# Performance work log

Hardware: AMD Instinct MI355X
Metric: run time of the kernel (lower is better)

Reference implementation:

```python
import jax, jax.numpy as jnp
import numpy as np

N = 10000        # nodes
E = 320000       # edges (avg degree 32)
IN = 739         # in_channels
C = 64           # hid_channels
H = 1            # heads
D = C // H       # per-head dim
L = 10           # layer_num
G = 64           # num graphs in batch
LAMBD = 1.0


def setup_inputs() -> dict:
    key = jax.random.key(0)
    ks = jax.random.split(key, 14)
    s = 0.05
    return {
        "x": jax.random.normal(ks[0], (N, IN), jnp.float32),
        "edge_index": jax.random.randint(ks[1], (2, E), 0, N, dtype=jnp.int32),
        "batch": jnp.sort(jax.random.randint(ks[2], (N,), 0, G, dtype=jnp.int32)),
        # InitFeat: Linear(739->64), ELU, Linear(64->64) (dropout = identity at eval)
        "w0": jax.random.normal(ks[3], (IN, C), jnp.float32) * s,
        "b0": jax.random.normal(ks[4], (C,), jnp.float32) * s,
        "w1": jax.random.normal(ks[5], (C, C), jnp.float32) * s,
        "b1": jax.random.normal(ks[6], (C,), jnp.float32) * s,
        # AeroConv attention vectors for k = 1..L-1
        "conv_att": jax.random.normal(ks[7], (L - 1, H, D), jnp.float32) * s,
        # UpdateZ k=0 (g = h, width D) and k=1..L-1 (g = [h, z_scale], width 2D)
        "hop_att0": jax.random.normal(ks[8], (H, D), jnp.float32) * s,
        "hop_bias0": jax.random.normal(ks[9], (H,), jnp.float32) * s,
        "hop_att": jax.random.normal(ks[10], (L - 1, H, 2 * D), jnp.float32) * s,
        "hop_bias": jax.random.normal(ks[11], (L - 1, H), jnp.float32) * s,
        # readout head Linear(64->1)
        "w_head": jax.random.normal(ks[12], (C, 1), jnp.float32) * s,
        "b_head": jax.random.normal(ks[13], (1,), jnp.float32) * s,
    }


def reference(x, edge_index, batch, w0, b0, w1, b1, conv_att,
              hop_att0, hop_bias0, hop_att, hop_bias, w_head, b_head):
    src, dst = edge_index[0], edge_index[1]

    # ---- InitFeat (dropout is identity at inference) ----
    h = x @ w0 + b0
    h = jax.nn.elu(h) @ w1 + b1              # [N, C]
    x = h

    # ---- UpdateZ, k = 0: z = h * hop_attention ----
    hh = x.reshape(N, H, D)
    attn = jnp.sum(hop_att0 * jax.nn.elu(hh), axis=-1) + hop_bias0   # [N, H]
    z = hh * attn[..., None]                 # [N, H, D]

    for i in range(L - 1):
        k = i + 1
        scale = jnp.float32(np.log(LAMBD / k + 1.0 + 1e-6))
        z_scale = z * scale                  # [N, H, D]

        # per-edge attention: elu(z_i + z_j), dot with att, softplus
        a = jax.nn.elu(z_scale[src] + z_scale[dst])                   # [E, H, D]
        a = jax.nn.softplus(jnp.sum(conv_att[i] * a, axis=-1)) + 1e-6  # [E, H]

        # symmetric normalization by scatter-summed degree
        adj_sum = jax.ops.segment_sum(a, dst, num_segments=N)         # [N, H]
        inv = jnp.maximum(adj_sum, 1e-32) ** -0.5
        na = (inv[src] * a * inv[dst])[..., None]                     # [E, H, 1]

        # weighted scatter-sum of source features
        msgs = x[src].reshape(E, H, D) * na                           # [E, H, D]
        x = jax.ops.segment_sum(msgs, dst, num_segments=N).reshape(N, C)

        # UpdateZ (k >= 1): g = [h, z_scale]
        hh = x.reshape(N, H, D)
        g = jnp.concatenate([hh, z_scale], axis=-1)                   # [N, H, 2D]
        attn = jnp.sum(hop_att[i] * jax.nn.elu(g), axis=-1) + hop_bias[i]
        z = z + hh * attn[..., None]

    # ---- readout: elu, global mean pool over batch, linear head ----
    zf = jax.nn.elu(z.reshape(N, C))
    seg_sum = jax.ops.segment_sum(zf, batch, num_segments=G)          # [G, C]
    cnt = jax.ops.segment_sum(jnp.ones((N,), zf.dtype), batch, num_segments=G)
    pooled = seg_sum / jnp.maximum(cnt, 1.0)[:, None]
    return pooled @ w_head + b_head                                   # [G, 1]
```

## Files before the change

### kernel.cpp

```cpp
#include <hip/hip_runtime.h>
#include <hip/hip_bf16.h>
#include <math.h>

#define NN     10000
#define EE     320000
#define IN_CH  739
#define CC     64
#define GG     64
#define NLAYER 9
#define NBUCK  157
#define CHUNK  2048

__device__ __forceinline__ float eluf(float x) {
    return x > 0.f ? x : __expf(x) - 1.f;
}
__device__ __forceinline__ float softplusf(float x) {
    return fmaxf(x, 0.f) + __logf(1.f + __expf(-fabsf(x)));
}
__device__ __forceinline__ float wave_sum(float v) {
#pragma unroll
    for (int off = 32; off > 0; off >>= 1) v += __shfl_xor(v, off, 64);
    return v;
}

__device__ __forceinline__ int swizzle2500(int b) {
    const int r = b & 7;
    const int q = b >> 3;
    return r * 312 + (r < 4 ? r : 4) + q;
}

__global__ __launch_bounds__(256) void k_gemm1_part(
    const float* __restrict__ x, const float* __restrict__ w0,
    float* __restrict__ hpart)
{
    __shared__ float xs[64 * 68];
    __shared__ float ws[64 * 64];
    const int tid = threadIdx.x;
    const int cg_ = tid & 15;
    const int rg = tid >> 4;
    const int split = blockIdx.x & 3;
    const int R0 = (blockIdx.x >> 2) * 64;
    const int K0 = split * 192;

    const int sk = tid & 63;
    const int sr = tid >> 6;

    float xr[16], wr[16];
    float acc[4][4] = {};

#pragma unroll
    for (int i = 0; i < 16; ++i) {
        const int r = sr + 4 * i;
        const int gr = R0 + r;
        const int gk = K0 + sk;
        xr[i] = (gr < NN && gk < IN_CH) ? x[(size_t)gr * IN_CH + gk] : 0.f;
        const int wk = K0 + r;
        wr[i] = (wk < IN_CH) ? w0[wk * CC + sk] : 0.f;
    }

    for (int t = 0; t < 3; ++t) {
        __syncthreads();
#pragma unroll
        for (int i = 0; i < 16; ++i) {
            const int r = sr + 4 * i;
            xs[r * 68 + sk] = xr[i];
            ws[r * 64 + sk] = wr[i];
        }
        __syncthreads();
        if (t + 1 < 3) {
            const int k0 = K0 + (t + 1) * 64;
#pragma unroll
            for (int i = 0; i < 16; ++i) {
                const int r = sr + 4 * i;
                const int gr = R0 + r;
                const int gk = k0 + sk;
                xr[i] = (gr < NN && gk < IN_CH) ? x[(size_t)gr * IN_CH + gk] : 0.f;
                const int wk = k0 + r;
                wr[i] = (wk < IN_CH) ? w0[wk * CC + sk] : 0.f;
            }
        }
#pragma unroll 4
        for (int k4 = 0; k4 < 64; k4 += 4) {
            float4 xv[4], wv[4];
#pragma unroll
            for (int j = 0; j < 4; ++j)
                xv[j] = *(const float4*)&xs[(rg * 4 + j) * 68 + k4];
#pragma unroll
            for (int q = 0; q < 4; ++q)
                wv[q] = *(const float4*)&ws[(k4 + q) * 64 + cg_ * 4];
#pragma unroll
            for (int j = 0; j < 4; ++j) {
                const float* xf = (const float*)&xv[j];
#pragma unroll
                for (int q = 0; q < 4; ++q) {
                    const float* wf = (const float*)&wv[q];
#pragma unroll
                    for (int i = 0; i < 4; ++i)
                        acc[j][i] = fmaf(xf[q], wf[i], acc[j][i]);
                }
            }
        }
    }

#pragma unroll
    for (int j = 0; j < 4; ++j) {
        const int row = R0 + rg * 4 + j;
        if (row < NN)
            *(float4*)&hpart[((size_t)split * NN + row) * CC + cg_ * 4] =
                make_float4(acc[j][0], acc[j][1], acc[j][2], acc[j][3]);
    }
}

__global__ __launch_bounds__(256) void k_init2(
    const float* __restrict__ hpart,
    const float* __restrict__ b0, const float* __restrict__ w1,
    const float* __restrict__ b1,
    const float* __restrict__ hop_att0, const float* __restrict__ hop_bias0,
    float scale1,
    float* __restrict__ xout, float* __restrict__ zout,
    float* __restrict__ zsout)
{
    __shared__ float xs[32 * 68];
    __shared__ float ws[64 * 64];
    const int tid = threadIdx.x;
    const int R0 = blockIdx.x * 32;

#pragma unroll
    for (int j = 0; j < 2; ++j) {
        const int slot = tid + 256 * j;
        const int row = slot >> 4;
        const int col4 = (slot & 15) * 4;
        const int grow = R0 + row;
        float4 s = make_float4(0.f, 0.f, 0.f, 0.f);
        if (grow < NN) {
#pragma unroll
            for (int sp = 0; sp < 4; ++sp) {
                const float4 v =
                    *(const float4*)&hpart[((size_t)sp * NN + grow) * CC + col4];
                s.x += v.x; s.y += v.y; s.z += v.z; s.w += v.w;
            }
        }
        const float4 bb = *(const float4*)&b0[col4];
        s.x = eluf(s.x + bb.x); s.y = eluf(s.y + bb.y);
        s.z = eluf(s.z + bb.z); s.w = eluf(s.w + bb.w);
        *(float4*)&xs[row * 68 + col4] = s;
    }
    {
        const int sk = tid & 63;
        const int sr = tid >> 6;
#pragma unroll
        for (int i = 0; i < 16; ++i)
            ws[(sr + 4 * i) * 64 + sk] = w1[(sr + 4 * i) * CC + sk];
    }
    __syncthreads();

    const int cg_ = tid & 15;
    const int rg = tid >> 4;
    float acc2[2][4];
    const float4 b1v = *(const float4*)&b1[cg_ * 4];
#pragma unroll
    for (int j = 0; j < 2; ++j) {
        acc2[j][0] = b1v.x; acc2[j][1] = b1v.y;
        acc2[j][2] = b1v.z; acc2[j][3] = b1v.w;
    }
#pragma unroll 4
    for (int k4 = 0; k4 < 64; k4 += 4) {
        float4 xv[2], wv[4];
#pragma unroll
        for (int j = 0; j < 2; ++j)
            xv[j] = *(const float4*)&xs[(rg * 2 + j) * 68 + k4];
#pragma unroll
        for (int q = 0; q < 4; ++q)
            wv[q] = *(const float4*)&ws[(k4 + q) * 64 + cg_ * 4];
#pragma unroll
        for (int j = 0; j < 2; ++j) {
            const float* xf = (const float*)&xv[j];
#pragma unroll
            for (int q = 0; q < 4; ++q) {
                const float* wf = (const float*)&wv[q];
#pragma unroll
                for (int i = 0; i < 4; ++i)
                    acc2[j][i] = fmaf(xf[q], wf[i], acc2[j][i]);
            }
        }
    }

    __syncthreads();
#pragma unroll
    for (int j = 0; j < 2; ++j)
        *(float4*)&ws[(rg * 2 + j) * 64 + cg_ * 4] =
            make_float4(acc2[j][0], acc2[j][1], acc2[j][2], acc2[j][3]);
    __syncthreads();

    const int c = tid & 63;
    const int w = tid >> 6;
    const float ha = hop_att0[c];
    const float hb = hop_bias0[0];
#pragma unroll
    for (int rr = 0; rr < 8; ++rr) {
        const int r = w * 8 + rr;
        const float v = ws[r * 64 + c];
        const float attn = wave_sum(ha * eluf(v)) + hb;
        const int row = R0 + r;
        if (row < NN) {
            const float zv = v * attn;
            xout[row * CC + c] = v;
            zout[row * CC + c] = zv;
            zsout[row * CC + c] = zv * scale1;
        }
    }
}

__global__ __launch_bounds__(256) void k_hist(const int* __restrict__ ei,
                                              int* __restrict__ deg)
{
    const int e = blockIdx.x * 256 + threadIdx.x;
    atomicAdd(&deg[ei[EE + e]], 1);
}

__global__ __launch_bounds__(256) void k_scan(const int* __restrict__ deg,
                                              int* __restrict__ offs,
                                              int* __restrict__ bcur)
{
    __shared__ int part[256];
    const int tid = threadIdx.x;
    const int start = tid * 40;
    const int end = start + 40 < NN ? start + 40 : NN;
    int sum = 0;
    for (int i = start; i < end; ++i) sum += deg[i];
    part[tid] = sum;
    __syncthreads();
    if (tid == 0) {
        int run = 0;
        for (int i = 0; i < 256; ++i) { int t = part[i]; part[i] = run; run += t; }
    }
    __syncthreads();
    int run = part[tid];
    for (int i = start; i < end; ++i) {
        offs[i] = run;
        if ((i & 63) == 0) bcur[i >> 6] = run;
        run += deg[i];
    }
}

__global__ __launch_bounds__(256) void k_part1(
    const int* __restrict__ ei, int* __restrict__ bcur,
    int2* __restrict__ csr_pair)
{
    __shared__ int hist[NBUCK];
    __shared__ int scan_s[NBUCK];
    __shared__ int base_g[NBUCK];
    __shared__ int lcur[NBUCK];
    __shared__ int2 staged[CHUNK];
    const int tid = threadIdx.x;
    const int e0 = blockIdx.x * CHUNK;

    for (int b = tid; b < NBUCK; b += 256) { hist[b] = 0; lcur[b] = 0; }
    __syncthreads();

    int src[8], dst[8];
#pragma unroll
    for (int j = 0; j < 8; ++j) {
        const int e = e0 + tid + 256 * j;
        if (e < EE) {
            src[j] = ei[e];
            dst[j] = ei[EE + e];
            atomicAdd(&hist[dst[j] >> 6], 1);
        } else dst[j] = -1;
    }
    __syncthreads();
    if (tid == 0) {
        int run = 0;
        for (int b = 0; b < NBUCK; ++b) { scan_s[b] = run; run += hist[b]; }
    }
    __syncthreads();
    if (tid < NBUCK && hist[tid] > 0)
        base_g[tid] = atomicAdd(&bcur[tid], hist[tid]);
    __syncthreads();
#pragma unroll
    for (int j = 0; j < 8; ++j) {
        if (dst[j] >= 0) {
            const int b = dst[j] >> 6;
            const int r = atomicAdd(&lcur[b], 1);
            staged[scan_s[b] + r] = make_int2(src[j], dst[j]);
        }
    }
    __syncthreads();
    const int tot = (EE - e0) < CHUNK ? (EE - e0) : CHUNK;
    for (int i = tid; i < tot; i += 256) {
        const int2 p = staged[i];
        const int b = p.y >> 6;
        csr_pair[base_g[b] + (i - scan_s[b])] = p;
    }
}

__global__ __launch_bounds__(256) void k_part2(
    const int* __restrict__ offs, const int2* __restrict__ csr_pair,
    int* __restrict__ csr_src)
{
    __shared__ int lcnt[64];
    __shared__ int loffs[64];
    const int b = blockIdx.x;
    const int tid = threadIdx.x;
    const int d0 = b * 64;
    if (tid < 64) {
        lcnt[tid] = 0;
        const int d = d0 + tid;
        loffs[tid] = (d < NN) ? offs[d] : EE;
    }
    __syncthreads();
    const int r0 = offs[d0];
    const int r1 = (d0 + 64 < NN) ? offs[d0 + 64] : EE;
    for (int i = r0 + tid; i < r1; i += 256) {
        const int2 p = csr_pair[i];
        const int ld = p.y & 63;
        const int r = atomicAdd(&lcnt[ld], 1);
        csr_src[loffs[ld] + r] = p.x;
    }
}

__global__ __launch_bounds__(256) void k_bounds(const int* __restrict__ batch,
                                                int* __restrict__ gstart)
{
    const int n = blockIdx.x * 256 + threadIdx.x;
    if (n >= NN) return;
    if (n == 0)
        for (int g = 0; g <= batch[0]; ++g) gstart[g] = 0;
    else {
        const int b0 = batch[n - 1], b1 = batch[n];
        for (int g = b0 + 1; g <= b1; ++g) gstart[g] = n;
    }
    if (n == NN - 1)
        for (int g = batch[NN - 1] + 1; g <= GG; ++g) gstart[g] = NN;
}

__global__ __launch_bounds__(256) void k_edge_adj(
    const int* __restrict__ offs, const int* __restrict__ deg,
    const int* __restrict__ csr_src,
    const float* __restrict__ zs_buf, const float* __restrict__ conv_att,
    float* __restrict__ a_csr, float* __restrict__ inv_adj)
{
    const int n = swizzle2500(blockIdx.x) * 4 + (threadIdx.x >> 6);
    const int lane = threadIdx.x & 63;
    const int l = lane & 15;
    const int grp = lane >> 4;
    const int start = offs[n];
    const int len = deg[n];

    const float4 zd = *(const float4*)(zs_buf + n * CC + l * 4);
    const float4 scv = *(const float4*)(conv_att + l * 4);

    float asum = 0.f;
    int i = grp;
    for (; i + 12 < len; i += 16) {
        const int s0 = csr_src[start + i];
        const int s1 = csr_src[start + i + 4];
        const int s2 = csr_src[start + i + 8];
        const int s3 = csr_src[start + i + 12];
        const float4 a0 = *(const float4*)(zs_buf + s0 * CC + l * 4);
        const float4 a1 = *(const float4*)(zs_buf + s1 * CC + l * 4);
        const float4 a2 = *(const float4*)(zs_buf + s2 * CC + l * 4);
        const float4 a3 = *(const float4*)(zs_buf + s3 * CC + l * 4);
        float p0 = scv.x * eluf(a0.x + zd.x);
        p0 = fmaf(scv.y, eluf(a0.y + zd.y), p0);
        p0 = fmaf(scv.z, eluf(a0.z + zd.z), p0);
        p0 = fmaf(scv.w, eluf(a0.w + zd.w), p0);
        float p1 = scv.x * eluf(a1.x + zd.x);
        p1 = fmaf(scv.y, eluf(a1.y + zd.y), p1);
        p1 = fmaf(scv.z, eluf(a1.z + zd.z), p1);
        p1 = fmaf(scv.w, eluf(a1.w + zd.w), p1);
        float p2 = scv.x * eluf(a2.x + zd.x);
        p2 = fmaf(scv.y, eluf(a2.y + zd.y), p2);
        p2 = fmaf(scv.z, eluf(a2.z + zd.z), p2);
        p2 = fmaf(scv.w, eluf(a2.w + zd.w), p2);
        float p3 = scv.x * eluf(a3.x + zd.x);
        p3 = fmaf(scv.y, eluf(a3.y + zd.y), p3);
        p3 = fmaf(scv.z, eluf(a3.z + zd.z), p3);
        p3 = fmaf(scv.w, eluf(a3.w + zd.w), p3);
#pragma unroll
        for (int off = 8; off > 0; off >>= 1) {
            p0 += __shfl_xor(p0, off, 64);
            p1 += __shfl_xor(p1, off, 64);
            p2 += __shfl_xor(p2, off, 64);
            p3 += __shfl_xor(p3, off, 64);
        }
        const float ae0 = softplusf(p0) + 1e-6f;
        const float ae1 = softplusf(p1) + 1e-6f;
        const float ae2 = softplusf(p2) + 1e-6f;
        const float ae3 = softplusf(p3) + 1e-6f;
        asum += ae0 + ae1 + ae2 + ae3;
        if (l == 0) {
            a_csr[start + i] = ae0;
            a_csr[start + i + 4] = ae1;
            a_csr[start + i + 8] = ae2;
            a_csr[start + i + 12] = ae3;
        }
    }
    for (; i < len; i += 4) {
        const int s0 = csr_src[start + i];
        const float4 a0 = *(const float4*)(zs_buf + s0 * CC + l * 4);
        float p0 = scv.x * eluf(a0.x + zd.x);
        p0 = fmaf(scv.y, eluf(a0.y + zd.y), p0);
        p0 = fmaf(scv.z, eluf(a0.z + zd.z), p0);
        p0 = fmaf(scv.w, eluf(a0.w + zd.w), p0);
#pragma unroll
        for (int off = 8; off > 0; off >>= 1) p0 += __shfl_xor(p0, off, 64);
        const float ae0 = softplusf(p0) + 1e-6f;
        asum += ae0;
        if (l == 0) a_csr[start + i] = ae0;
    }

    asum += __shfl_xor(asum, 16, 64);
    asum += __shfl_xor(asum, 32, 64);
    if (lane == 0) inv_adj[n] = rsqrtf(fmaxf(asum, 1e-32f));
}

__global__ __launch_bounds__(256) void k_msg_fused(
    const int* __restrict__ offs, const int* __restrict__ deg,
    const int* __restrict__ csr_src, const float* __restrict__ a_csr,
    const float* __restrict__ inv_adj, const float* __restrict__ x,
    float* __restrict__ xn, float* __restrict__ z,
    float* __restrict__ zs_buf,
    const float* __restrict__ hop_att, const float* __restrict__ hop_bias,
    float scale_next)
{
    const int n = swizzle2500(blockIdx.x) * 4 + (threadIdx.x >> 6);
    const int lane = threadIdx.x & 63;
    const int l = lane & 15;
    const int grp = lane >> 4;
    const int start = offs[n];
    const int len = deg[n];
    const float invd = inv_adj[n];
    const float4* x4 = (const float4*)x;

    float4 acc = make_float4(0.f, 0.f, 0.f, 0.f);
    int i = grp;
    for (; i + 4 < len; i += 8) {
        const int s0 = csr_src[start + i];
        const int s1 = csr_src[start + i + 4];
        const float na0 = a_csr[start + i] * inv_adj[s0] * invd;
        const float na1 = a_csr[start + i + 4] * inv_adj[s1] * invd;
        const float4 v0 = x4[s0 * 16 + l];
        const float4 v1 = x4[s1 * 16 + l];
        acc.x = fmaf(v0.x, na0, acc.x);
        acc.y = fmaf(v0.y, na0, acc.y);
        acc.z = fmaf(v0.z, na0, acc.z);
        acc.w = fmaf(v0.w, na0, acc.w);
        acc.x = fmaf(v1.x, na1, acc.x);
        acc.y = fmaf(v1.y, na1, acc.y);
        acc.z = fmaf(v1.z, na1, acc.z);
        acc.w = fmaf(v1.w, na1, acc.w);
    }
    for (; i < len; i += 4) {
        const int s0 = csr_src[start + i];
        const float na0 = a_csr[start + i] * inv_adj[s0] * invd;
        const float4 v0 = x4[s0 * 16 + l];
        acc.x = fmaf(v0.x, na0, acc.x);
        acc.y = fmaf(v0.y, na0, acc.y);
        acc.z = fmaf(v0.z, na0, acc.z);
        acc.w = fmaf(v0.w, na0, acc.w);
    }

    acc.x += __shfl_xor(acc.x, 16, 64);
    acc.y += __shfl_xor(acc.y, 16, 64);
    acc.z += __shfl_xor(acc.z, 16, 64);
    acc.w += __shfl_xor(acc.w, 16, 64);
    acc.x += __shfl_xor(acc.x, 32, 64);
    acc.y += __shfl_xor(acc.y, 32, 64);
    acc.z += __shfl_xor(acc.z, 32, 64);
    acc.w += __shfl_xor(acc.w, 32, 64);

    const float4 zv  = *(const float4*)(z + n * CC + l * 4);
    const float4 zsv = *(const float4*)(zs_buf + n * CC + l * 4);
    const float4 ha  = *(const float4*)(hop_att + l * 4);
    const float4 hz  = *(const float4*)(hop_att + CC + l * 4);
    float gp = ha.x * eluf(acc.x) + ha.y * eluf(acc.y)
             + ha.z * eluf(acc.z) + ha.w * eluf(acc.w)
             + hz.x * eluf(zsv.x) + hz.y * eluf(zsv.y)
             + hz.z * eluf(zsv.z) + hz.w * eluf(zsv.w);
#pragma unroll
    for (int off = 8; off > 0; off >>= 1) gp += __shfl_xor(gp, off, 64);
    const float attn = gp + hop_bias[0];

    if (lane < 16) {
        float4 znew;
        znew.x = fmaf(acc.x, attn, zv.x);
        znew.y = fmaf(acc.y, attn, zv.y);
        znew.z = fmaf(acc.z, attn, zv.z);
        znew.w = fmaf(acc.w, attn, zv.w);
        *(float4*)(z + n * CC + l * 4) = znew;
        *(float4*)(zs_buf + n * CC + l * 4) =
            make_float4(znew.x * scale_next, znew.y * scale_next,
                        znew.z * scale_next, znew.w * scale_next);
        *(float4*)(xn + n * CC + l * 4) = acc;
    }
}

__global__ __launch_bounds__(256) void k_pool_head(
    const float* __restrict__ z, const int* __restrict__ gstart,
    const float* __restrict__ w_head, const float* __restrict__ b_head,
    float* __restrict__ out)
{
    __shared__ float red[4][CC];
    const int g = blockIdx.x;
    const int w = threadIdx.x >> 6;
    const int c = threadIdx.x & 63;
    const int s0 = gstart[g], s1 = gstart[g + 1];

    float acc = 0.f;
    for (int n = s0 + w; n < s1; n += 4) acc += eluf(z[n * CC + c]);
    red[w][c] = acc;
    __syncthreads();
    if (w == 0) {
        const float v = red[0][c] + red[1][c] + red[2][c] + red[3][c];
        const float tot = wave_sum(v * w_head[c]);
        if (c == 0)
            out[g] = tot / fmaxf((float)(s1 - s0), 1.f) + b_head[0];
    }
}

extern "C" void kernel_launch(void* const* d_in, const int* in_sizes, int n_in,
                              void* d_out, int out_size, void* d_ws, size_t ws_size,
                              hipStream_t stream) {
    const float* x        = (const float*)d_in[0];
    const int*   ei       = (const int*)d_in[1];
    const int*   batch    = (const int*)d_in[2];
    const float* w0       = (const float*)d_in[3];
    const float* b0       = (const float*)d_in[4];
    const float* w1       = (const float*)d_in[5];
    const float* b1       = (const float*)d_in[6];
    const float* conv_att = (const float*)d_in[7];
    const float* hop_att0 = (const float*)d_in[8];
    const float* hop_bias0= (const float*)d_in[9];
    const float* hop_att  = (const float*)d_in[10];
    const float* hop_bias = (const float*)d_in[11];
    const float* w_head   = (const float*)d_in[12];
    const float* b_head   = (const float*)d_in[13];
    float* out = (float*)d_out;

    float sc[NLAYER + 2];
    for (int k = 1; k <= NLAYER; ++k)
        sc[k] = (float)log(1.0 / (double)k + 1.0 + 1e-6);
    sc[NLAYER + 1] = 0.f;

    float* xA      = (float*)d_ws;
    float* xB      = xA + NN * CC;
    float* zbuf    = xB + NN * CC;
    float* zsbuf   = zbuf + NN * CC;
    float* inv_adj = zsbuf + NN * CC;
    float* hpart   = inv_adj + NN;
    float* a_csr   = hpart;
    int*   csr_src = (int*)(a_csr + EE);
    int2*  csr_pair= (int2*)(csr_src + EE);
    int*   deg     = (int*)(csr_pair + EE);
    int*   offs    = deg + NN;
    int*   bcur    = offs + NN;
    int*   gstart  = bcur + NBUCK;

    k_gemm1_part<<<157 * 4, 256, 0, stream>>>(x, w0, hpart);
    k_init2<<<313, 256, 0, stream>>>(hpart, b0, w1, b1, hop_att0, hop_bias0,
                                     sc[1], xA, zbuf, zsbuf);

    hipMemsetAsync(deg, 0, (size_t)NN * 4, stream);
    k_hist<<<EE / 256, 256, 0, stream>>>(ei, deg);
    k_scan<<<1, 256, 0, stream>>>(deg, offs, bcur);
    k_part1<<<(EE + CHUNK - 1) / CHUNK, 256, 0, stream>>>(ei, bcur, csr_pair);
    k_part2<<<NBUCK, 256, 0, stream>>>(offs, csr_pair, csr_src);
    k_bounds<<<(NN + 255) / 256, 256, 0, stream>>>(batch, gstart);

    float* xcur = xA;
    float* xnext = xB;
    for (int i = 0; i < NLAYER; ++i) {
        const float scale_next = (i + 1 < NLAYER) ? sc[i + 2] : 0.f;
        k_edge_adj<<<NN / 4, 256, 0, stream>>>(offs, deg, csr_src, zsbuf,
                                               conv_att + i * CC,
                                               a_csr, inv_adj);
        k_msg_fused<<<NN / 4, 256, 0, stream>>>(offs, deg, csr_src, a_csr,
                                                inv_adj, xcur, xnext, zbuf,
                                                zsbuf,
                                                hop_att + i * 2 * CC,
                                                hop_bias + i, scale_next);
        float* t = xcur; xcur = xnext; xnext = t;
    }

    k_pool_head<<<GG, 256, 0, stream>>>(zbuf, gstart, w_head, b_head, out);
}
```

Before: 446.7 us.

## Pre-scale source features by inverse degree norm and process four nodes per wave

The edge-attention kernel now also writes y = x * inv_adj per node, so the message kernel no longer gathers inv_adj[src] per edge and applies inv_adj[dst] once after the reduction. Both kernels loop over four nodes per wave with a quarter of the blocks, which hoists the attention-vector loads. The block swizzle is dropped and the x ping-pong buffers become a single x/y pair. This removes one random scalar gather per edge and adds an extra N×64 write and read per layer.

```diff
diff --git a/kernel.cpp b/kernel.cpp
--- a/kernel.cpp
+++ b/kernel.cpp
@@ -21,12 +21,6 @@
 #pragma unroll
     for (int off = 32; off > 0; off >>= 1) v += __shfl_xor(v, off, 64);
     return v;
-}
-
-__device__ __forceinline__ int swizzle2500(int b) {
-    const int r = b & 7;
-    const int q = b >> 3;
-    return r * 312 + (r < 4 ? r : 4) + q;
 }
 
 __global__ __launch_bounds__(256) void k_gemm1_part(
@@ -338,161 +332,177 @@
     const int* __restrict__ offs, const int* __restrict__ deg,
     const int* __restrict__ csr_src,
     const float* __restrict__ zs_buf, const float* __restrict__ conv_att,
-    float* __restrict__ a_csr, float* __restrict__ inv_adj)
-{
-    const int n = swizzle2500(blockIdx.x) * 4 + (threadIdx.x >> 6);
+    const float* __restrict__ x,
+    float* __restrict__ a_csr, float* __restrict__ inv_adj,
+    float* __restrict__ y)
+{
+    const int wv = blockIdx.x * 4 + (threadIdx.x >> 6);
     const int lane = threadIdx.x & 63;
     const int l = lane & 15;
     const int grp = lane >> 4;
-    const int start = offs[n];
-    const int len = deg[n];
-
-    const float4 zd = *(const float4*)(zs_buf + n * CC + l * 4);
     const float4 scv = *(const float4*)(conv_att + l * 4);
 
-    float asum = 0.f;
-    int i = grp;
-    for (; i + 12 < len; i += 16) {
-        const int s0 = csr_src[start + i];
-        const int s1 = csr_src[start + i + 4];
-        const int s2 = csr_src[start + i + 8];
-        const int s3 = csr_src[start + i + 12];
-        const float4 a0 = *(const float4*)(zs_buf + s0 * CC + l * 4);
-        const float4 a1 = *(const float4*)(zs_buf + s1 * CC + l * 4);
-        const float4 a2 = *(const float4*)(zs_buf + s2 * CC + l * 4);
-        const float4 a3 = *(const float4*)(zs_buf + s3 * CC + l * 4);
-        float p0 = scv.x * eluf(a0.x + zd.x);
-        p0 = fmaf(scv.y, eluf(a0.y + zd.y), p0);
-        p0 = fmaf(scv.z, eluf(a0.z + zd.z), p0);
-        p0 = fmaf(scv.w, eluf(a0.w + zd.w), p0);
-        float p1 = scv.x * eluf(a1.x + zd.x);
-        p1 = fmaf(scv.y, eluf(a1.y + zd.y), p1);
-        p1 = fmaf(scv.z, eluf(a1.z + zd.z), p1);
-        p1 = fmaf(scv.w, eluf(a1.w + zd.w), p1);
-        float p2 = scv.x * eluf(a2.x + zd.x);
-        p2 = fmaf(scv.y, eluf(a2.y + zd.y), p2);
-        p2 = fmaf(scv.z, eluf(a2.z + zd.z), p2);
-        p2 = fmaf(scv.w, eluf(a2.w + zd.w), p2);
-        float p3 = scv.x * eluf(a3.x + zd.x);
-        p3 = fmaf(scv.y, eluf(a3.y + zd.y), p3);
-        p3 = fmaf(scv.z, eluf(a3.z + zd.z), p3);
-        p3 = fmaf(scv.w, eluf(a3.w + zd.w), p3);
-#pragma unroll
-        for (int off = 8; off > 0; off >>= 1) {
-            p0 += __shfl_xor(p0, off, 64);
-            p1 += __shfl_xor(p1, off, 64);
-            p2 += __shfl_xor(p2, off, 64);
-            p3 += __shfl_xor(p3, off, 64);
-        }
-        const float ae0 = softplusf(p0) + 1e-6f;
-        const float ae1 = softplusf(p1) + 1e-6f;
-        const float ae2 = softplusf(p2) + 1e-6f;
-        const float ae3 = softplusf(p3) + 1e-6f;
-        asum += ae0 + ae1 + ae2 + ae3;
-        if (l == 0) {
-            a_csr[start + i] = ae0;
-            a_csr[start + i + 4] = ae1;
-            a_csr[start + i + 8] = ae2;
-            a_csr[start + i + 12] = ae3;
-        }
-    }
-    for (; i < len; i += 4) {
-        const int s0 = csr_src[start + i];
-        const float4 a0 = *(const float4*)(zs_buf + s0 * CC + l * 4);
-        float p0 = scv.x * eluf(a0.x + zd.x);
-        p0 = fmaf(scv.y, eluf(a0.y + zd.y), p0);
-        p0 = fmaf(scv.z, eluf(a0.z + zd.z), p0);
-        p0 = fmaf(scv.w, eluf(a0.w + zd.w), p0);
-#pragma unroll
-        for (int off = 8; off > 0; off >>= 1) p0 += __shfl_xor(p0, off, 64);
-        const float ae0 = softplusf(p0) + 1e-6f;
-        asum += ae0;
-        if (l == 0) a_csr[start + i] = ae0;
-    }
-
-    asum += __shfl_xor(asum, 16, 64);
-    asum += __shfl_xor(asum, 32, 64);
-    if (lane == 0) inv_adj[n] = rsqrtf(fmaxf(asum, 1e-32f));
+#pragma unroll
+    for (int t = 0; t < 4; ++t) {
+        const int n = wv * 4 + t;
+        const int start = offs[n];
+        const int len = deg[n];
+        const float4 zd = *(const float4*)(zs_buf + n * CC + l * 4);
+
+        float asum = 0.f;
+        int i = grp;
+        for (; i + 12 < len; i += 16) {
+            const int s0 = csr_src[start + i];
+            const int s1 = csr_src[start + i + 4];
+            const int s2 = csr_src[start + i + 8];
+            const int s3 = csr_src[start + i + 12];
+            const float4 a0 = *(const float4*)(zs_buf + s0 * CC + l * 4);
+            const float4 a1 = *(const float4*)(zs_buf + s1 * CC + l * 4);
+            const float4 a2 = *(const float4*)(zs_buf + s2 * CC + l * 4);
+            const float4 a3 = *(const float4*)(zs_buf + s3 * CC + l * 4);
+            float p0 = scv.x * eluf(a0.x + zd.x);
+            p0 = fmaf(scv.y, eluf(a0.y + zd.y), p0);
+            p0 = fmaf(scv.z, eluf(a0.z + zd.z), p0);
+            p0 = fmaf(scv.w, eluf(a0.w + zd.w), p0);
+            float p1 = scv.x * eluf(a1.x + zd.x);
+            p1 = fmaf(scv.y, eluf(a1.y + zd.y), p1);
+            p1 = fmaf(scv.z, eluf(a1.z + zd.z), p1);
+            p1 = fmaf(scv.w, eluf(a1.w + zd.w), p1);
+            float p2 = scv.x * eluf(a2.x + zd.x);
+            p2 = fmaf(scv.y, eluf(a2.y + zd.y), p2);
+            p2 = fmaf(scv.z, eluf(a2.z + zd.z), p2);
+            p2 = fmaf(scv.w, eluf(a2.w + zd.w), p2);
+            float p3 = scv.x * eluf(a3.x + zd.x);
+            p3 = fmaf(scv.y, eluf(a3.y + zd.y), p3);
+            p3 = fmaf(scv.z, eluf(a3.z + zd.z), p3);
+            p3 = fmaf(scv.w, eluf(a3.w + zd.w), p3);
+#pragma unroll
+            for (int off = 8; off > 0; off >>= 1) {
+                p0 += __shfl_xor(p0, off, 64);
+                p1 += __shfl_xor(p1, off, 64);
+                p2 += __shfl_xor(p2, off, 64);
+                p3 += __shfl_xor(p3, off, 64);
+            }
+            const float ae0 = softplusf(p0) + 1e-6f;
+            const float ae1 = softplusf(p1) + 1e-6f;
+            const float ae2 = softplusf(p2) + 1e-6f;
+            const float ae3 = softplusf(p3) + 1e-6f;
+            asum += ae0 + ae1 + ae2 + ae3;
+            if (l == 0) {
+                a_csr[start + i] = ae0;
+                a_csr[start + i + 4] = ae1;
+                a_csr[start + i + 8] = ae2;
+                a_csr[start + i + 12] = ae3;
+            }
+        }
+        for (; i < len; i += 4) {
+            const int s0 = csr_src[start + i];
+            const float4 a0 = *(const float4*)(zs_buf + s0 * CC + l * 4);
+            float p0 = scv.x * eluf(a0.x + zd.x);
+            p0 = fmaf(scv.y, eluf(a0.y + zd.y), p0);
+            p0 = fmaf(scv.z, eluf(a0.z + zd.z), p0);
+            p0 = fmaf(scv.w, eluf(a0.w + zd.w), p0);
+#pragma unroll
+            for (int off = 8; off > 0; off >>= 1) p0 += __shfl_xor(p0, off, 64);
+            const float ae0 = softplusf(p0) + 1e-6f;
+            asum += ae0;
+            if (l == 0) a_csr[start + i] = ae0;
+        }
+
+        asum += __shfl_xor(asum, 16, 64);
+        asum += __shfl_xor(asum, 32, 64);
+        const float inv = rsqrtf(fmaxf(asum, 1e-32f));
+        if (lane == 0) inv_adj[n] = inv;
+        y[n * CC + lane] = x[n * CC + lane] * inv;
+    }
 }
 
 __global__ __launch_bounds__(256) void k_msg_fused(
     const int* __restrict__ offs, const int* __restrict__ deg,
     const int* __restrict__ csr_src, const float* __restrict__ a_csr,
-    const float* __restrict__ inv_adj, const float* __restrict__ x,
-    float* __restrict__ xn, float* __restrict__ z,
+    const float* __restrict__ inv_adj, const float* __restrict__ y,
+    float* __restrict__ x, float* __restrict__ z,
     float* __restrict__ zs_buf,
     const float* __restrict__ hop_att, const float* __restrict__ hop_bias,
     float scale_next)
 {
-    const int n = swizzle2500(blockIdx.x) * 4 + (threadIdx.x >> 6);
+    const int wv = blockIdx.x * 4 + (threadIdx.x >> 6);
     const int lane = threadIdx.x & 63;
     const int l = lane & 15;
     const int grp = lane >> 4;
-    const int start = offs[n];
-    const int len = deg[n];
-    const float invd = inv_adj[n];
-    const float4* x4 = (const float4*)x;
-
-    float4 acc = make_float4(0.f, 0.f, 0.f, 0.f);
-    int i = grp;
-    for (; i + 4 < len; i += 8) {
-        const int s0 = csr_src[start + i];
-        const int s1 = csr_src[start + i + 4];
-        const float na0 = a_csr[start + i] * inv_adj[s0] * invd;
-        const float na1 = a_csr[start + i + 4] * inv_adj[s1] * invd;
-        const float4 v0 = x4[s0 * 16 + l];
-        const float4 v1 = x4[s1 * 16 + l];
-        acc.x = fmaf(v0.x, na0, acc.x);
-        acc.y = fmaf(v0.y, na0, acc.y);
-        acc.z = fmaf(v0.z, na0, acc.z);
-        acc.w = fmaf(v0.w, na0, acc.w);
-        acc.x = fmaf(v1.x, na1, acc.x);
-        acc.y = fmaf(v1.y, na1, acc.y);
-        acc.z = fmaf(v1.z, na1, acc.z);
-        acc.w = fmaf(v1.w, na1, acc.w);
-    }
-    for (; i < len; i += 4) {
-        const int s0 = csr_src[start + i];
-        const float na0 = a_csr[start + i] * inv_adj[s0] * invd;
-        const float4 v0 = x4[s0 * 16 + l];
-        acc.x = fmaf(v0.x, na0, acc.x);
-        acc.y = fmaf(v0.y, na0, acc.y);
-        acc.z = fmaf(v0.z, na0, acc.z);
-        acc.w = fmaf(v0.w, na0, acc.w);
-    }
-
-    acc.x += __shfl_xor(acc.x, 16, 64);
-    acc.y += __shfl_xor(acc.y, 16, 64);
-    acc.z += __shfl_xor(acc.z, 16, 64);
-    acc.w += __shfl_xor(acc.w, 16, 64);
-    acc.x += __shfl_xor(acc.x, 32, 64);
-    acc.y += __shfl_xor(acc.y, 32, 64);
-    acc.z += __shfl_xor(acc.z, 32, 64);
-    acc.w += __shfl_xor(acc.w, 32, 64);
-
-    const float4 zv  = *(const float4*)(z + n * CC + l * 4);
-    const float4 zsv = *(const float4*)(zs_buf + n * CC + l * 4);
-    const float4 ha  = *(const float4*)(hop_att + l * 4);
-    const float4 hz  = *(const float4*)(hop_att + CC + l * 4);
-    float gp = ha.x * eluf(acc.x) + ha.y * eluf(acc.y)
-             + ha.z * eluf(acc.z) + ha.w * eluf(acc.w)
-             + hz.x * eluf(zsv.x) + hz.y * eluf(zsv.y)
-             + hz.z * eluf(zsv.z) + hz.w * eluf(zsv.w);
-#pragma unroll
-    for (int off = 8; off > 0; off >>= 1) gp += __shfl_xor(gp, off, 64);
-    const float attn = gp + hop_bias[0];
-
-    if (lane < 16) {
-        float4 znew;
-        znew.x = fmaf(acc.x, attn, zv.x);
-        znew.y = fmaf(acc.y, attn, zv.y);
-        znew.z = fmaf(acc.z, attn, zv.z);
-        znew.w = fmaf(acc.w, attn, zv.w);
-        *(float4*)(z + n * CC + l * 4) = znew;
-        *(float4*)(zs_buf + n * CC + l * 4) =
-            make_float4(znew.x * scale_next, znew.y * scale_next,
-                        znew.z * scale_next, znew.w * scale_next);
-        *(float4*)(xn + n * CC + l * 4) = acc;
+    const float4* y4 = (const float4*)y;
+    const float4 ha = *(const float4*)(hop_att + l * 4);
+    const float4 hz = *(const float4*)(hop_att + CC + l * 4);
+    const float hb = hop_bias[0];
+
+#pragma unroll
+    for (int t = 0; t < 4; ++t) {
+        const int n = wv * 4 + t;
+        const int start = offs[n];
+        const int len = deg[n];
+        const float invd = inv_adj[n];
+
+        float4 acc = make_float4(0.f, 0.f, 0.f, 0.f);
+        int i = grp;
+        for (; i + 4 < len; i += 8) {
+            const int s0 = csr_src[start + i];
+            const int s1 = csr_src[start + i + 4];
+            const float na0 = a_csr[start + i];
+            const float na1 = a_csr[start + i + 4];
+            const float4 v0 = y4[s0 * 16 + l];
+            const float4 v1 = y4[s1 * 16 + l];
+            acc.x = fmaf(v0.x, na0, acc.x);
+            acc.y = fmaf(v0.y, na0, acc.y);
+            acc.z = fmaf(v0.z, na0, acc.z);
+            acc.w = fmaf(v0.w, na0, acc.w);
+            acc.x = fmaf(v1.x, na1, acc.x);
+            acc.y = fmaf(v1.y, na1, acc.y);
+            acc.z = fmaf(v1.z, na1, acc.z);
+            acc.w = fmaf(v1.w, na1, acc.w);
+        }
+        for (; i < len; i += 4) {
+            const int s0 = csr_src[start + i];
+            const float na0 = a_csr[start + i];
+            const float4 v0 = y4[s0 * 16 + l];
+            acc.x = fmaf(v0.x, na0, acc.x);
+            acc.y = fmaf(v0.y, na0, acc.y);
+            acc.z = fmaf(v0.z, na0, acc.z);
+            acc.w = fmaf(v0.w, na0, acc.w);
+        }
+
+        acc.x += __shfl_xor(acc.x, 16, 64);
+        acc.y += __shfl_xor(acc.y, 16, 64);
+        acc.z += __shfl_xor(acc.z, 16, 64);
+        acc.w += __shfl_xor(acc.w, 16, 64);
+        acc.x += __shfl_xor(acc.x, 32, 64);
+        acc.y += __shfl_xor(acc.y, 32, 64);
+        acc.z += __shfl_xor(acc.z, 32, 64);
+        acc.w += __shfl_xor(acc.w, 32, 64);
+
+        acc.x *= invd; acc.y *= invd; acc.z *= invd; acc.w *= invd;
+
+        const float4 zv  = *(const float4*)(z + n * CC + l * 4);
+        const float4 zsv = *(const float4*)(zs_buf + n * CC + l * 4);
+        float gp = ha.x * eluf(acc.x) + ha.y * eluf(acc.y)
+                 + ha.z * eluf(acc.z) + ha.w * eluf(acc.w)
+                 + hz.x * eluf(zsv.x) + hz.y * eluf(zsv.y)
+                 + hz.z * eluf(zsv.z) + hz.w * eluf(zsv.w);
+#pragma unroll
+        for (int off = 8; off > 0; off >>= 1) gp += __shfl_xor(gp, off, 64);
+        const float attn = gp + hb;
+
+        if (lane < 16) {
+            float4 znew;
+            znew.x = fmaf(acc.x, attn, zv.x);
+            znew.y = fmaf(acc.y, attn, zv.y);
+            znew.z = fmaf(acc.z, attn, zv.z);
+            znew.w = fmaf(acc.w, attn, zv.w);
+            *(float4*)(z + n * CC + l * 4) = znew;
+            *(float4*)(zs_buf + n * CC + l * 4) =
+                make_float4(znew.x * scale_next, znew.y * scale_next,
+                            znew.z * scale_next, znew.w * scale_next);
+            *(float4*)(x + n * CC + l * 4) = acc;
+        }
     }
 }
 
@@ -522,7 +532,7 @@
 extern "C" void kernel_launch(void* const* d_in, const int* in_sizes, int n_in,
                               void* d_out, int out_size, void* d_ws, size_t ws_size,
                               hipStream_t stream) {
-    const float* x        = (const float*)d_in[0];
+    const float* x_in     = (const float*)d_in[0];
     const int*   ei       = (const int*)d_in[1];
     const int*   batch    = (const int*)d_in[2];
     const float* w0       = (const float*)d_in[3];
@@ -543,9 +553,9 @@
         sc[k] = (float)log(1.0 / (double)k + 1.0 + 1e-6);
     sc[NLAYER + 1] = 0.f;
 
-    float* xA      = (float*)d_ws;
-    float* xB      = xA + NN * CC;
-    float* zbuf    = xB + NN * CC;
+    float* xbuf    = (float*)d_ws;
+    float* ybuf    = xbuf + NN * CC;
+    float* zbuf    = ybuf + NN * CC;
     float* zsbuf   = zbuf + NN * CC;
     float* inv_adj = zsbuf + NN * CC;
     float* hpart   = inv_adj + NN;
@@ -557,9 +567,9 @@
     int*   bcur    = offs + NN;
     int*   gstart  = bcur + NBUCK;
 
-    k_gemm1_part<<<157 * 4, 256, 0, stream>>>(x, w0, hpart);
+    k_gemm1_part<<<157 * 4, 256, 0, stream>>>(x_in, w0, hpart);
     k_init2<<<313, 256, 0, stream>>>(hpart, b0, w1, b1, hop_att0, hop_bias0,
-                                     sc[1], xA, zbuf, zsbuf);
+                                     sc[1], xbuf, zbuf, zsbuf);
 
     hipMemsetAsync(deg, 0, (size_t)NN * 4, stream);
     k_hist<<<EE / 256, 256, 0, stream>>>(ei, deg);
@@ -568,19 +578,16 @@
     k_part2<<<NBUCK, 256, 0, stream>>>(offs, csr_pair, csr_src);
     k_bounds<<<(NN + 255) / 256, 256, 0, stream>>>(batch, gstart);
 
-    float* xcur = xA;
-    float* xnext = xB;
     for (int i = 0; i < NLAYER; ++i) {
         const float scale_next = (i + 1 < NLAYER) ? sc[i + 2] : 0.f;
-        k_edge_adj<<<NN / 4, 256, 0, stream>>>(offs, deg, csr_src, zsbuf,
-                                               conv_att + i * CC,
-                                               a_csr, inv_adj);
-        k_msg_fused<<<NN / 4, 256, 0, stream>>>(offs, deg, csr_src, a_csr,
-                                                inv_adj, xcur, xnext, zbuf,
-                                                zsbuf,
-                                                hop_att + i * 2 * CC,
-                                                hop_bias + i, scale_next);
-        float* t = xcur; xcur = xnext; xnext = t;
+        k_edge_adj<<<NN / 16, 256, 0, stream>>>(offs, deg, csr_src, zsbuf,
+                                                conv_att + i * CC, xbuf,
+                                                a_csr, inv_adj, ybuf);
+        k_msg_fused<<<NN / 16, 256, 0, stream>>>(offs, deg, csr_src, a_csr,
+                                                 inv_adj, ybuf, xbuf, zbuf,
+                                                 zsbuf,
+                                                 hop_att + i * 2 * CC,
+                                                 hop_bias + i, scale_next);
     }
 
     k_pool_head<<<GG, 256, 0, stream>>>(zbuf, gstart, w_head, b_head, out);
```

After: 580.4 us. +29.9%, slower.
